# Optimization experiments

Measured on AMD Instinct MI355X. Metric: run time of the kernel, lower is better.

## Reference

```python
import jax, jax.numpy as jnp
import numpy as np

B, S, D, H = 2, 2048, 1024, 16
HD = D // H
NEG = -9000000000000000.0


def setup_inputs() -> dict:
    key = jax.random.key(0)
    ks = jax.random.split(key, 12)
    scale = 1.0 / np.sqrt(D)
    inp = {
        "k": jax.random.normal(ks[0], (B, S, D), jnp.float32),
        "q": jax.random.normal(ks[1], (B, S, D), jnp.float32),
        "v": jax.random.normal(ks[2], (B, S, D), jnp.float32),
        # causal mask, float (0/1), shape [B, 1, S, S] as expected by __call__
        "mask": jnp.broadcast_to(jnp.tril(jnp.ones((S, S), jnp.float32))[None, None], (B, 1, S, S)),
        "Wq": jax.random.normal(ks[3], (D, D), jnp.float32) * scale,
        "bq": jnp.zeros((D,), jnp.float32),
        "Wk": jax.random.normal(ks[4], (D, D), jnp.float32) * scale,
        "bk": jnp.zeros((D,), jnp.float32),
        "Wv": jax.random.normal(ks[5], (D, D), jnp.float32) * scale,
        "bv": jnp.zeros((D,), jnp.float32),
        "Wo": jax.random.normal(ks[6], (D, D), jnp.float32) * scale,
        "bo": jnp.zeros((D,), jnp.float32),
    }
    return inp


def _split_heads(x):
    # [B, S, D] -> [B, H, S, HD]
    return x.reshape(B, S, H, HD).transpose(0, 2, 1, 3)


def reference(k, q, v, mask, Wq, bq, Wk, bk, Wv, bv, Wo, bo):
    keys = _split_heads(k @ Wk + bk)
    queries = _split_heads(q @ Wq + bq)
    values = _split_heads(v @ Wv + bv)
    # scaled dot product with materialized scores (faithful to source)
    logits = jnp.einsum("bhqd,bhkd->bhqk", queries, keys) / np.sqrt(HD)
    logits = jnp.where(mask == 0, NEG, logits)
    attention = jax.nn.softmax(logits, axis=-1)
    out = jnp.einsum("bhqk,bhkd->bhqd", attention, values)
    out = out.transpose(0, 2, 1, 3).reshape(B, S, D)
    o = out @ Wo + bo
    return (o, attention)
```

## Files before the change

kernel.cpp:

```cpp
#include <hip/hip_runtime.h>
#include <stdint.h>

typedef unsigned short u16;
typedef short short8 __attribute__((ext_vector_type(8)));
typedef unsigned short ushort8 __attribute__((ext_vector_type(8)));
typedef unsigned short us4 __attribute__((ext_vector_type(4)));
typedef float f32x4 __attribute__((ext_vector_type(4)));

#define S_LEN 2048
#define D_DIM 1024
#define H_NUM 16
#define HD_DIM 64

__device__ __forceinline__ float bf2f(u16 u) {
  union { uint32_t i; float f; } x; x.i = ((uint32_t)u) << 16; return x.f;
}
__device__ __forceinline__ u16 f2bf(float f) {
  union { float f; uint32_t i; } x; x.f = f;
  uint32_t u = x.i;
  uint32_t r = (u + 0x7fffu + ((u >> 16) & 1u)) >> 16;
  return (u16)r;
}
__device__ __forceinline__ f32x4 mfma16(short8 a, short8 b, f32x4 c) {
  return __builtin_amdgcn_mfma_f32_16x16x32_bf16(a, b, c, 0, 0, 0);
}
__device__ __forceinline__ bool mask_is_f32(const void* mask) {
  return *(const float*)mask == 1.0f;
}
__device__ __forceinline__ void async_cp16(const u16* g, u16* l) {
  __builtin_amdgcn_global_load_lds((const __attribute__((address_space(1))) unsigned int*)g,
                                   (__attribute__((address_space(3))) unsigned int*)l,
                                   16, 0, 0);
}

__global__ __launch_bounds__(256) void prep(const void* __restrict__ q,
                                            const void* __restrict__ k,
                                            const void* __restrict__ v,
                                            const void* __restrict__ w0,
                                            const void* __restrict__ w1,
                                            const void* __restrict__ w2,
                                            const void* __restrict__ w3,
                                            const void* __restrict__ b0,
                                            const void* __restrict__ b1,
                                            const void* __restrict__ b2,
                                            const void* __restrict__ b3,
                                            u16* __restrict__ Cb,
                                            u16* __restrict__ WT,
                                            float* __restrict__ biasF,
                                            const void* __restrict__ mask) {
  __shared__ u16 t[64][65];
  bool isf32 = mask_is_f32(mask);
  int bid = blockIdx.x;
  int tid = threadIdx.x;
  if (bid < 6144) {
    int z = bid >> 11;
    const void* src = (z == 0) ? q : (z == 1) ? k : v;
    size_t i = ((size_t)(bid & 2047) * 256 + tid) * 8;
    u16* dst = Cb + (size_t)z * 4194304;
    if (isf32) {
      const f32x4* p = (const f32x4*)((const float*)src + i);
      f32x4 a = p[0], b = p[1];
      ushort8 o;
#pragma unroll
      for (int j = 0; j < 4; j++) { o[j] = f2bf(a[j]); o[4 + j] = f2bf(b[j]); }
      *(ushort8*)(dst + i) = o;
    } else {
      *(ushort8*)(dst + i) = *(const ushort8*)((const u16*)src + i);
    }
  } else if (bid < 7168) {
    int t2 = bid - 6144;
    int y = t2 >> 8, tile = t2 & 255;
    const void* W = (y == 0) ? w0 : (y == 1) ? w1 : (y == 2) ? w2 : w3;
    u16* out = WT + (size_t)y * 1048576;
    int r0 = (tile >> 4) * 64, c0 = (tile & 15) * 64;
    int rr = tid >> 6, cc = tid & 63;
#pragma unroll
    for (int i = 0; i < 16; i++) {
      int r = i * 4 + rr;
      size_t idx = (size_t)(r0 + r) * 1024 + c0 + cc;
      t[r][cc] = isf32 ? f2bf(((const float*)W)[idx]) : ((const u16*)W)[idx];
    }
    __syncthreads();
#pragma unroll
    for (int i = 0; i < 16; i++) {
      int r = i * 4 + rr;
      out[(size_t)(c0 + r) * 1024 + r0 + cc] = t[cc][r];
    }
  } else {
    int t3 = bid - 7168;
    int y = t3 >> 2;
    const void* b = (y == 0) ? b0 : (y == 1) ? b1 : (y == 2) ? b2 : b3;
    int i = (t3 & 3) * 256 + tid;
    biasF[y * 1024 + i] = isf32 ? ((const float*)b)[i] : bf2f(((const u16*)b)[i]);
  }
}

__global__ __launch_bounds__(256) void v_transpose(const u16* __restrict__ V,
                                                   u16* __restrict__ Vt) {
  __shared__ u16 t[64][65];
  int bh = blockIdx.x, st = blockIdx.y;
  int b = bh >> 4, h = bh & 15;
  int tid = threadIdx.x;
  int rr = tid >> 6, cc = tid & 63;
#pragma unroll
  for (int i = 0; i < 16; i++) {
    int r = i * 4 + rr;
    t[r][cc] = V[(size_t)(b * S_LEN + st * 64 + r) * D_DIM + h * HD_DIM + cc];
  }
  __syncthreads();
#pragma unroll
  for (int i = 0; i < 16; i++) {
    int r = i * 4 + rr;
    Vt[(size_t)(bh * HD_DIM + r) * S_LEN + st * 64 + cc] = t[cc][r];
  }
}

__device__ __forceinline__ void gemm_body(const u16* __restrict__ A,
                                          const u16* __restrict__ Bt,
                                          const float* __restrict__ bias,
                                          void* __restrict__ C, bool cf32,
                                          int M, int N, int K, int m0, int n0,
                                          u16* lds) {
  u16* lA = lds;
  u16* lB = lds + 8192;
  int tid = threadIdx.x;
  int lane = tid & 63, w = tid >> 6;
  int wr = w >> 1, wc = w & 1;
  f32x4 acc[4][4] = {};
  const int nk = K >> 5;
  int grow = lane >> 2, gcol = (lane & 3) * 8;

#define GEMM_ISSUE(kt, buf)                                                              \
  {                                                                                      \
    _Pragma("unroll") for (int p = 0; p < 2; p++) {                                      \
      async_cp16(A + (size_t)(m0 + p * 64 + w * 16 + grow) * K + (kt) * 32 + gcol,       \
                 &lA[(buf) * 4096 + p * 2048 + w * 512]);                                \
      async_cp16(Bt + (size_t)(n0 + p * 64 + w * 16 + grow) * K + (kt) * 32 + gcol,      \
                 &lB[(buf) * 4096 + p * 2048 + w * 512]);                                \
    }                                                                                    \
  }

  GEMM_ISSUE(0, 0);
  __syncthreads();
  int cur = 0;
  for (int kt = 0; kt < nk; kt++) {
    if (kt + 1 < nk) GEMM_ISSUE(kt + 1, cur ^ 1);
    short8 af[4], bf[4];
#pragma unroll
    for (int i = 0; i < 4; i++) {
      af[i] = *(const short8*)(&lA[cur * 4096 + (wr * 64 + i * 16 + (lane & 15)) * 32 + (lane >> 4) * 8]);
      bf[i] = *(const short8*)(&lB[cur * 4096 + (wc * 64 + i * 16 + (lane & 15)) * 32 + (lane >> 4) * 8]);
    }
#pragma unroll
    for (int i = 0; i < 4; i++)
#pragma unroll
      for (int j = 0; j < 4; j++)
        acc[i][j] = mfma16(af[i], bf[j], acc[i][j]);
    __syncthreads();
    cur ^= 1;
  }
#undef GEMM_ISSUE
#pragma unroll
  for (int j = 0; j < 4; j++) {
    float bv = bias[n0 + wc * 64 + j * 16 + (lane & 15)];
#pragma unroll
    for (int i = 0; i < 4; i++) {
#pragma unroll
      for (int jj = 0; jj < 4; jj++) {
        int row = m0 + wr * 64 + i * 16 + ((lane >> 4) << 2) + jj;
        int col = n0 + wc * 64 + j * 16 + (lane & 15);
        float val = acc[i][j][jj] + bv;
        if (cf32) ((float*)C)[(size_t)row * N + col] = val;
        else ((u16*)C)[(size_t)row * N + col] = f2bf(val);
      }
    }
  }
}

__global__ __launch_bounds__(256, 2) void qkv_gemm(const u16* __restrict__ Ab,
                                                   const u16* __restrict__ WTall,
                                                   const float* __restrict__ biasF,
                                                   u16* __restrict__ outbase) {
  __shared__ __align__(16) u16 smem[16384];
  int z = blockIdx.z;
  gemm_body(Ab + (size_t)z * 4194304, WTall + (size_t)z * 1048576, biasF + z * 1024,
            outbase + (size_t)z * 4194304, false,
            4096, 1024, 1024, blockIdx.y * 128, blockIdx.x * 128, smem);
}

__global__ __launch_bounds__(256, 3) void attn_flash(const u16* __restrict__ Qg,
                                                     const u16* __restrict__ Kg,
                                                     const u16* __restrict__ VtG,
                                                     u16* __restrict__ ctx,
                                                     float* __restrict__ statsI) {
  int x = blockIdx.x, bh = blockIdx.y;
  int b = bh >> 4, h = bh & 15;
  int tid = threadIdx.x, lane = tid & 63, w = tid >> 6;
  __shared__ __align__(16) u16 lK[2][64 * 72];
  __shared__ __align__(16) u16 lV[2][64 * 72];
  __shared__ __align__(16) u16 lP[4][16 * 72];
  u16* lPw = &lP[w][0];
  int sr = tid >> 3, sc8 = (tid & 7) * 8;

  for (int s = 0; s < 2; s++) {
    int qt = (s == 0) ? x : 31 - x;
    int q0 = qt * 64;
    int nkv = qt + 1;
    int qrow = q0 + w * 16 + (lane & 15);

    short8 qf[2];
#pragma unroll
    for (int ks = 0; ks < 2; ks++)
      qf[ks] = *(const short8*)(Qg + (size_t)(b * S_LEN + qrow) * D_DIM +
                                h * HD_DIM + ks * 32 + (lane >> 4) * 8);

    ushort8 kreg[2], vreg[2];
    auto loadK = [&](int kt) {
#pragma unroll
      for (int p = 0; p < 2; p++)
        kreg[p] = *(const ushort8*)(Kg + (size_t)(b * S_LEN + kt * 64 + p * 32 + sr) * D_DIM +
                                    h * HD_DIM + sc8);
    };
    auto writeK = [&](int buf) {
#pragma unroll
      for (int p = 0; p < 2; p++)
        *(ushort8*)(&lK[buf][(p * 32 + sr) * 72 + sc8]) = kreg[p];
    };
    auto loadV = [&](int kt) {
#pragma unroll
      for (int p = 0; p < 2; p++)
        vreg[p] = *(const ushort8*)(VtG + (size_t)(bh * HD_DIM + p * 32 + sr) * S_LEN +
                                    kt * 64 + sc8);
    };
    auto writeV = [&](int buf) {
#pragma unroll
      for (int p = 0; p < 2; p++)
        *(ushort8*)(&lV[buf][(p * 32 + sr) * 72 + sc8]) = vreg[p];
    };

    float l_ = 0.f;
    f32x4 oacc[4] = {};

    loadK(0); loadV(0); writeK(0); writeV(0);
    __syncthreads();
    int cur = 0;
    for (int kt = 0; kt < nkv; kt++) {
      if (kt + 1 < nkv) { loadK(kt + 1); loadV(kt + 1); }
      f32x4 sc[4];
#pragma unroll
      for (int j = 0; j < 4; j++) {
        short8 kf0 = *(const short8*)(&lK[cur][(j * 16 + (lane & 15)) * 72 + (lane >> 4) * 8]);
        short8 kf1 = *(const short8*)(&lK[cur][(j * 16 + (lane & 15)) * 72 + 32 + (lane >> 4) * 8]);
        f32x4 a = {0.f, 0.f, 0.f, 0.f};
        a = mfma16(kf0, qf[0], a);
        a = mfma16(kf1, qf[1], a);
        sc[j] = a;
      }
      bool needmask = (kt == qt);
      float ss = 0.f;
#pragma unroll
      for (int j = 0; j < 4; j++) {
        us4 pb;
#pragma unroll
        for (int jj = 0; jj < 4; jj++) {
          float p = __expf(sc[j][jj] * 0.125f);
          if (needmask) {
            int kv = kt * 64 + j * 16 + ((lane >> 4) << 2) + jj;
            if (kv > qrow) p = 0.f;
          }
          ss += p;
          pb[jj] = f2bf(p);
        }
        *(us4*)(&lPw[(lane & 15) * 72 + j * 16 + ((lane >> 4) << 2)]) = pb;
      }
      ss += __shfl_xor(ss, 16);
      ss += __shfl_xor(ss, 32);
      l_ += ss;
      short8 pa[2];
#pragma unroll
      for (int ks = 0; ks < 2; ks++)
        pa[ks] = *(const short8*)(&lPw[(lane & 15) * 72 + ks * 32 + (lane >> 4) * 8]);
#pragma unroll
      for (int f = 0; f < 4; f++) {
        short8 vb0 = *(const short8*)(&lV[cur][(f * 16 + (lane & 15)) * 72 + (lane >> 4) * 8]);
        short8 vb1 = *(const short8*)(&lV[cur][(f * 16 + (lane & 15)) * 72 + 32 + (lane >> 4) * 8]);
        oacc[f] = mfma16(pa[0], vb0, oacc[f]);
        oacc[f] = mfma16(pa[1], vb1, oacc[f]);
      }
      if (kt + 1 < nkv) { writeK(cur ^ 1); writeV(cur ^ 1); }
      __syncthreads();
      cur ^= 1;
    }

    float invl = 1.f / l_;
    float io[4];
#pragma unroll
    for (int jj = 0; jj < 4; jj++) io[jj] = __shfl(invl, ((lane >> 4) << 2) + jj);
#pragma unroll
    for (int f = 0; f < 4; f++)
#pragma unroll
      for (int jj = 0; jj < 4; jj++) {
        int row = q0 + w * 16 + ((lane >> 4) << 2) + jj;
        int col = h * HD_DIM + f * 16 + (lane & 15);
        ctx[(size_t)(b * S_LEN + row) * D_DIM + col] = f2bf(oacc[f][jj] * io[jj]);
      }
    if (lane < 16) statsI[(size_t)bh * S_LEN + qrow] = invl;
  }
}

__global__ __launch_bounds__(256, 2) void tail_fused(const u16* __restrict__ ctx,
                                                     const u16* __restrict__ WoT,
                                                     const float* __restrict__ biasO,
                                                     const u16* __restrict__ Qg,
                                                     const u16* __restrict__ Kg,
                                                     const float* __restrict__ statsI,
                                                     void* __restrict__ dout,
                                                     const void* __restrict__ mask) {
  __shared__ __align__(16) u16 smem[16384];
  bool isf32 = mask_is_f32(mask);
  int bid = blockIdx.x;
  int tid = threadIdx.x, lane = tid & 63, w = tid >> 6;

  if (bid < 256) {
    gemm_body(ctx, WoT, biasO, dout, isf32,
              4096, 1024, 1024, (bid >> 3) * 128, (bid & 7) * 128, smem);
    return;
  }

  int pb = bid - 256;
  int x = pb & 15, bh = pb >> 4;
  int b = bh >> 4, h = bh & 15;
  float* attnF = (float*)dout + 4194304;
  u16* attnB = (u16*)dout + 4194304;
  int sr = tid >> 3, sc8 = (tid & 7) * 8;

  for (int s = 0; s < 2; s++) {
    int qt = (s == 0) ? x : 31 - x;
    int q0 = qt * 64;
    int nkv = qt + 1;
    int qrow = q0 + w * 16 + (lane & 15);

    short8 qf[2];
#pragma unroll
    for (int ks = 0; ks < 2; ks++)
      qf[ks] = *(const short8*)(Qg + (size_t)(b * S_LEN + qrow) * D_DIM +
                                h * HD_DIM + ks * 32 + (lane >> 4) * 8);
    float invl = statsI[(size_t)bh * S_LEN + qrow];

    ushort8 kreg[2];
    auto loadK = [&](int kt) {
#pragma unroll
      for (int p = 0; p < 2; p++)
        kreg[p] = *(const ushort8*)(Kg + (size_t)(b * S_LEN + kt * 64 + p * 32 + sr) * D_DIM +
                                    h * HD_DIM + sc8);
    };
    auto writeK = [&](int buf) {
#pragma unroll
      for (int p = 0; p < 2; p++)
        *(ushort8*)(&smem[buf * 4608 + (p * 32 + sr) * 72 + sc8]) = kreg[p];
    };

    loadK(0); writeK(0);
    __syncthreads();
    int cur = 0;
    for (int kt = 0; kt < nkv; kt++) {
      if (kt + 1 < nkv) loadK(kt + 1);
      bool needmask = (kt == qt);
#pragma unroll
      for (int j = 0; j < 4; j++) {
        short8 kf0 = *(const short8*)(&smem[cur * 4608 + (j * 16 + (lane & 15)) * 72 + (lane >> 4) * 8]);
        short8 kf1 = *(const short8*)(&smem[cur * 4608 + (j * 16 + (lane & 15)) * 72 + 32 + (lane >> 4) * 8]);
        f32x4 a = {0.f, 0.f, 0.f, 0.f};
        a = mfma16(kf0, qf[0], a);
        a = mfma16(kf1, qf[1], a);
        f32x4 p4;
        us4 pbv;
#pragma unroll
        for (int jj = 0; jj < 4; jj++) {
          float p = __expf(a[jj] * 0.125f) * invl;
          if (needmask) {
            int kv = kt * 64 + j * 16 + ((lane >> 4) << 2) + jj;
            if (kv > qrow) p = 0.f;
          }
          p4[jj] = p;
          pbv[jj] = f2bf(p);
        }
        size_t goff = ((size_t)bh * S_LEN + qrow) * S_LEN + kt * 64 + j * 16 + ((lane >> 4) << 2);
        if (isf32) *(f32x4*)(attnF + goff) = p4;
        else *(us4*)(attnB + goff) = pbv;
      }
      if (kt + 1 < nkv) writeK(cur ^ 1);
      __syncthreads();
      cur ^= 1;
    }

    {
      int z0 = nkv * 64;
      if (isf32) {
        int zc4 = (S_LEN - z0) >> 2;
        if (zc4 > 0) {
          f32x4 zz = {0.f, 0.f, 0.f, 0.f};
          for (int r = tid >> 5; r < 64; r += 8)
            for (int c = tid & 31; c < zc4; c += 32)
              *(f32x4*)(attnF + ((size_t)bh * S_LEN + q0 + r) * S_LEN + z0 + c * 4) = zz;
        }
      } else {
        int zc8 = (S_LEN - z0) >> 3;
        if (zc8 > 0) {
          ushort8 zz = {0, 0, 0, 0, 0, 0, 0, 0};
          for (int r = tid >> 5; r < 64; r += 8)
            for (int c = tid & 31; c < zc8; c += 32)
              *(ushort8*)(attnB + ((size_t)bh * S_LEN + q0 + r) * S_LEN + z0 + c * 8) = zz;
        }
      }
    }
  }
}

extern "C" void kernel_launch(void* const* d_in, const int* in_sizes, int n_in,
                              void* d_out, int out_size, void* d_ws, size_t ws_size,
                              hipStream_t stream) {
  const void* kin = d_in[0];
  const void* qin = d_in[1];
  const void* vin = d_in[2];
  const void* mask = d_in[3];
  const void* Wq = d_in[4];
  const void* bq = d_in[5];
  const void* Wk = d_in[6];
  const void* bk = d_in[7];
  const void* Wv = d_in[8];
  const void* bv = d_in[9];
  const void* Wo = d_in[10];
  const void* bo = d_in[11];

  u16* ws = (u16*)d_ws;
  u16* WT = ws;
  float* biasF = (float*)(ws + 4 * 1048576);
  u16* Cb = ws + 4 * 1048576 + 8192;
  u16* Qp = Cb + 3 * 4194304;
  u16* Kp = Qp + 4194304;
  u16* Vp = Kp + 4194304;
  u16* Vt = Vp + 4194304;
  u16* ctx = Vt + 4194304;
  float* statsI = (float*)(ctx + 4194304);

  prep<<<7184, 256, 0, stream>>>(qin, kin, vin, Wq, Wk, Wv, Wo, bq, bk, bv, bo,
                                 Cb, WT, biasF, mask);
  qkv_gemm<<<dim3(8, 32, 3), 256, 0, stream>>>(Cb, WT, biasF, Qp);
  v_transpose<<<dim3(32, 32), 256, 0, stream>>>(Vp, Vt);
  attn_flash<<<dim3(16, 32), 256, 0, stream>>>(Qp, Kp, Vt, ctx, statsI);
  tail_fused<<<768, 256, 0, stream>>>(ctx, WT + 3 * 1048576, biasF + 3072,
                                      Qp, Kp, statsI, d_out, mask);
}
```

Baseline: 282.9 us.

## Fuse V transpose into QKV GEMM epilogue and use nontemporal attention stores

Removes the separate v_transpose kernel: the V projection's GEMM epilogue now writes its output directly in the head-major transposed layout that attention expects, packing four bf16 values per store. This drops one kernel launch and a full read and write of the V activations. The attention-probability writes and zero-fill stores in the tail kernel become nontemporal stores to avoid polluting cache. Launch bounds for qkv_gemm and tail_fused rise from 2 to 3 blocks per SM, which may add register pressure or spills.

```diff
diff --git a/kernel.cpp b/kernel.cpp
--- a/kernel.cpp
+++ b/kernel.cpp
@@ -95,32 +95,12 @@
   }
 }
 
-__global__ __launch_bounds__(256) void v_transpose(const u16* __restrict__ V,
-                                                   u16* __restrict__ Vt) {
-  __shared__ u16 t[64][65];
-  int bh = blockIdx.x, st = blockIdx.y;
-  int b = bh >> 4, h = bh & 15;
-  int tid = threadIdx.x;
-  int rr = tid >> 6, cc = tid & 63;
-#pragma unroll
-  for (int i = 0; i < 16; i++) {
-    int r = i * 4 + rr;
-    t[r][cc] = V[(size_t)(b * S_LEN + st * 64 + r) * D_DIM + h * HD_DIM + cc];
-  }
-  __syncthreads();
-#pragma unroll
-  for (int i = 0; i < 16; i++) {
-    int r = i * 4 + rr;
-    Vt[(size_t)(bh * HD_DIM + r) * S_LEN + st * 64 + cc] = t[cc][r];
-  }
-}
-
 __device__ __forceinline__ void gemm_body(const u16* __restrict__ A,
                                           const u16* __restrict__ Bt,
                                           const float* __restrict__ bias,
-                                          void* __restrict__ C, bool cf32,
-                                          int M, int N, int K, int m0, int n0,
-                                          u16* lds) {
+                                          void* __restrict__ C, int mode,
+                                          int m0, int n0, u16* lds) {
+  const int K = 1024, N = 1024;
   u16* lA = lds;
   u16* lB = lds + 8192;
   int tid = threadIdx.x;
@@ -162,30 +142,40 @@
 #undef GEMM_ISSUE
 #pragma unroll
   for (int j = 0; j < 4; j++) {
-    float bv = bias[n0 + wc * 64 + j * 16 + (lane & 15)];
+    int col = n0 + wc * 64 + j * 16 + (lane & 15);
+    float bv = bias[col];
 #pragma unroll
     for (int i = 0; i < 4; i++) {
-#pragma unroll
-      for (int jj = 0; jj < 4; jj++) {
-        int row = m0 + wr * 64 + i * 16 + ((lane >> 4) << 2) + jj;
-        int col = n0 + wc * 64 + j * 16 + (lane & 15);
-        float val = acc[i][j][jj] + bv;
-        if (cf32) ((float*)C)[(size_t)row * N + col] = val;
-        else ((u16*)C)[(size_t)row * N + col] = f2bf(val);
-      }
-    }
-  }
-}
-
-__global__ __launch_bounds__(256, 2) void qkv_gemm(const u16* __restrict__ Ab,
+      int row0 = m0 + wr * 64 + i * 16 + ((lane >> 4) << 2);
+      if (mode == 2) {
+        int bb = row0 >> 11, s = row0 & 2047;
+        int h = col >> 6, hd = col & 63;
+        us4 pv;
+#pragma unroll
+        for (int jj = 0; jj < 4; jj++) pv[jj] = f2bf(acc[i][j][jj] + bv);
+        *(us4*)((u16*)C + (((size_t)(bb * 16 + h) * 64 + hd) << 11) + s) = pv;
+      } else {
+#pragma unroll
+        for (int jj = 0; jj < 4; jj++) {
+          float val = acc[i][j][jj] + bv;
+          if (mode == 1) ((float*)C)[(size_t)(row0 + jj) * N + col] = val;
+          else ((u16*)C)[(size_t)(row0 + jj) * N + col] = f2bf(val);
+        }
+      }
+    }
+  }
+}
+
+__global__ __launch_bounds__(256, 3) void qkv_gemm(const u16* __restrict__ Ab,
                                                    const u16* __restrict__ WTall,
                                                    const float* __restrict__ biasF,
-                                                   u16* __restrict__ outbase) {
+                                                   u16* __restrict__ QKbase,
+                                                   u16* __restrict__ Vt) {
   __shared__ __align__(16) u16 smem[16384];
   int z = blockIdx.z;
+  void* C = (z == 2) ? (void*)Vt : (void*)(QKbase + (size_t)z * 4194304);
   gemm_body(Ab + (size_t)z * 4194304, WTall + (size_t)z * 1048576, biasF + z * 1024,
-            outbase + (size_t)z * 4194304, false,
-            4096, 1024, 1024, blockIdx.y * 128, blockIdx.x * 128, smem);
+            C, (z == 2) ? 2 : 0, blockIdx.y * 128, blockIdx.x * 128, smem);
 }
 
 __global__ __launch_bounds__(256, 3) void attn_flash(const u16* __restrict__ Qg,
@@ -308,7 +298,7 @@
   }
 }
 
-__global__ __launch_bounds__(256, 2) void tail_fused(const u16* __restrict__ ctx,
+__global__ __launch_bounds__(256, 3) void tail_fused(const u16* __restrict__ ctx,
                                                      const u16* __restrict__ WoT,
                                                      const float* __restrict__ biasO,
                                                      const u16* __restrict__ Qg,
@@ -322,8 +312,8 @@
   int tid = threadIdx.x, lane = tid & 63, w = tid >> 6;
 
   if (bid < 256) {
-    gemm_body(ctx, WoT, biasO, dout, isf32,
-              4096, 1024, 1024, (bid >> 3) * 128, (bid & 7) * 128, smem);
+    gemm_body(ctx, WoT, biasO, dout, isf32 ? 1 : 0,
+              (bid >> 3) * 128, (bid & 7) * 128, smem);
     return;
   }
 
@@ -386,8 +376,8 @@
           pbv[jj] = f2bf(p);
         }
         size_t goff = ((size_t)bh * S_LEN + qrow) * S_LEN + kt * 64 + j * 16 + ((lane >> 4) << 2);
-        if (isf32) *(f32x4*)(attnF + goff) = p4;
-        else *(us4*)(attnB + goff) = pbv;
+        if (isf32) __builtin_nontemporal_store(p4, (f32x4*)(attnF + goff));
+        else __builtin_nontemporal_store(pbv, (us4*)(attnB + goff));
       }
       if (kt + 1 < nkv) writeK(cur ^ 1);
       __syncthreads();
@@ -402,7 +392,7 @@
           f32x4 zz = {0.f, 0.f, 0.f, 0.f};
           for (int r = tid >> 5; r < 64; r += 8)
             for (int c = tid & 31; c < zc4; c += 32)
-              *(f32x4*)(attnF + ((size_t)bh * S_LEN + q0 + r) * S_LEN + z0 + c * 4) = zz;
+              __builtin_nontemporal_store(zz, (f32x4*)(attnF + ((size_t)bh * S_LEN + q0 + r) * S_LEN + z0 + c * 4));
         }
       } else {
         int zc8 = (S_LEN - z0) >> 3;
@@ -410,7 +400,7 @@
           ushort8 zz = {0, 0, 0, 0, 0, 0, 0, 0};
           for (int r = tid >> 5; r < 64; r += 8)
             for (int c = tid & 31; c < zc8; c += 32)
-              *(ushort8*)(attnB + ((size_t)bh * S_LEN + q0 + r) * S_LEN + z0 + c * 8) = zz;
+              __builtin_nontemporal_store(zz, (ushort8*)(attnB + ((size_t)bh * S_LEN + q0 + r) * S_LEN + z0 + c * 8));
         }
       }
     }
@@ -439,15 +429,13 @@
   u16* Cb = ws + 4 * 1048576 + 8192;
   u16* Qp = Cb + 3 * 4194304;
   u16* Kp = Qp + 4194304;
-  u16* Vp = Kp + 4194304;
-  u16* Vt = Vp + 4194304;
+  u16* Vt = Kp + 4194304;
   u16* ctx = Vt + 4194304;
   float* statsI = (float*)(ctx + 4194304);
 
   prep<<<7184, 256, 0, stream>>>(qin, kin, vin, Wq, Wk, Wv, Wo, bq, bk, bv, bo,
                                  Cb, WT, biasF, mask);
-  qkv_gemm<<<dim3(8, 32, 3), 256, 0, stream>>>(Cb, WT, biasF, Qp);
-  v_transpose<<<dim3(32, 32), 256, 0, stream>>>(Vp, Vt);
+  qkv_gemm<<<dim3(8, 32, 3), 256, 0, stream>>>(Cb, WT, biasF, Qp, Vt);
   attn_flash<<<dim3(16, 32), 256, 0, stream>>>(Qp, Kp, Vt, ctx, statsI);
   tail_fused<<<768, 256, 0, stream>>>(ctx, WT + 3 * 1048576, biasF + 3072,
                                       Qp, Kp, statsI, d_out, mask);
```

Result: no change. 281.2 us (-0.6%).
